# Kernel tuning notes

Measured on AMD Instinct MI355X. Metric: run time of the kernel, lower is better.

Reference implementation:

```python
import jax, jax.numpy as jnp
import numpy as np

EPS = 1e-12  # F.normalize default eps (norm clamped to at least eps)


def setup_inputs() -> dict:
    key = jax.random.key(0)
    k1, k2, k3, k4 = jax.random.split(key, 4)
    B, Cin, Cout, H, W = 8, 128, 32, 256, 256
    x = jax.random.normal(k1, (B, Cin, H, W), dtype=jnp.float32)
    qk = jax.random.normal(k2, (B, 2 * Cout, H, W), dtype=jnp.float32)
    # 1x1 conv params (PyTorch Conv2d default init scale ~ 1/sqrt(fan_in))
    w_v = jax.random.normal(k3, (Cout, Cin), dtype=jnp.float32) / np.sqrt(Cin)
    b_v = jax.random.normal(k4, (Cout,), dtype=jnp.float32) / np.sqrt(Cin)
    temperature = jnp.ones((1, 1, 1), dtype=jnp.float32)
    return {"x": x, "qk": qk, "w_v": w_v, "b_v": b_v, "temperature": temperature}


def reference(x, qk, w_v, b_v, temperature):
    B, Cin, H, W = x.shape
    Co = w_v.shape[0]
    N = H * W
    # 1x1 conv == channel GEMM
    v = jnp.einsum('bchw,oc->bohw', x, w_v) + b_v[None, :, None, None]
    # split qk: k = first Co channels, q = last Co channels; head=1
    q = qk[:, Co:].reshape(B, 1, Co, N)
    k = qk[:, :Co].reshape(B, 1, Co, N)
    v = v.reshape(B, 1, Co, N)
    # L2-normalize over spatial dim (F.normalize: divide by max(norm, eps))
    q = q / jnp.maximum(jnp.linalg.norm(q, axis=-1, keepdims=True), EPS)
    k = k / jnp.maximum(jnp.linalg.norm(k, axis=-1, keepdims=True), EPS)
    # channel-wise (transposed) attention: [B,1,Co,Co]
    attn = jnp.einsum('bhcn,bhdn->bhcd', q, k) * temperature
    attn = jax.nn.softmax(attn, axis=-1)
    out = jnp.einsum('bhcd,bhdn->bhcn', attn, v)  # [B,1,Co,N]
    return out
```

## Files before the change

### kernel.cpp

```cpp
#include <hip/hip_runtime.h>
#include <hip/hip_bf16.h>
#include <math.h>

#define NB    8
#define CIN   128
#define CO    32
#define CH    64
#define NN    65536
#define CPB   512
#define GBLK  (NN/CPB)
#define TCOLS 128
#define NTILES (CPB/TCOLS)

typedef __attribute__((ext_vector_type(8))) short bf16x8;
typedef __attribute__((ext_vector_type(16))) float f32x16;

__device__ __forceinline__ short f2bf(float f) {
    union { __hip_bfloat16 h; short s; } u;
    u.h = __float2bfloat16(f);
    return u.s;
}
__device__ __forceinline__ float bf2f(short s) {
    union { __hip_bfloat16 h; short s; } u;
    u.s = s;
    return __bfloat162float(u.h);
}

__global__ __launch_bounds__(256) void gram_kernel(const float* __restrict__ qk,
                                                   float* __restrict__ part,
                                                   float* __restrict__ partsq) {
    __shared__ float smem[CH * TCOLS];
    float4* tile4 = (float4*)smem;

    const int b = blockIdx.y;
    const int blk = blockIdx.x;
    const int t = threadIdx.x;
    const int w = t >> 6;
    const int l = t & 63;
    const int c = l & 31;
    const int half = l >> 5;

    const float* qkb = qk + (size_t)b * CH * NN;
    const size_t colbase0 = (size_t)blk * CPB;

    const int lrow[8] = {  (t) >> 5, (t + 256) >> 5, (t + 512) >> 5, (t + 768) >> 5,
                           (t + 1024) >> 5, (t + 1280) >> 5, (t + 1536) >> 5, (t + 1792) >> 5 };
    const int lcol4 = t & 31;

    f32x16 acc = {};
    float sq[8] = {0.f, 0.f, 0.f, 0.f, 0.f, 0.f, 0.f, 0.f};

    float4 st[8];
#pragma unroll
    for (int k = 0; k < 8; ++k)
        st[k] = *(const float4*)(qkb + (size_t)lrow[k] * NN + colbase0 + lcol4 * 4);

#pragma unroll
    for (int tau = 0; tau < NTILES; ++tau) {
#pragma unroll
        for (int k = 0; k < 8; ++k) {
            float4 v = st[k];
            sq[k] = fmaf(v.x, v.x, sq[k]);
            sq[k] = fmaf(v.y, v.y, sq[k]);
            sq[k] = fmaf(v.z, v.z, sq[k]);
            sq[k] = fmaf(v.w, v.w, sq[k]);
            tile4[lrow[k] * 32 + (lcol4 ^ (lrow[k] & 7))] = v;
        }
        __syncthreads();

        if (tau + 1 < NTILES) {
            const size_t colbase = colbase0 + (size_t)(tau + 1) * TCOLS;
#pragma unroll
            for (int k = 0; k < 8; ++k)
                st[k] = *(const float4*)(qkb + (size_t)lrow[k] * NN + colbase + lcol4 * 4);
        }

#pragma unroll
        for (int ss = 0; ss < 2; ++ss) {
            const int s = 2 * w + ss;
            const int f0 = s * 4 + half * 2;
            const int qrow = CO + c;
            const int krow = c;
            const int sw = c & 7;
            float4 q0 = tile4[qrow * 32 + (f0 ^ sw)];
            float4 q1 = tile4[qrow * 32 + ((f0 + 1) ^ sw)];
            float4 k0 = tile4[krow * 32 + (f0 ^ sw)];
            float4 k1 = tile4[krow * 32 + ((f0 + 1) ^ sw)];

            float qf[8] = {q0.x, q0.y, q0.z, q0.w, q1.x, q1.y, q1.z, q1.w};
            float kf[8] = {k0.x, k0.y, k0.z, k0.w, k1.x, k1.y, k1.z, k1.w};

            bf16x8 ah, al, bh, bl;
#pragma unroll
            for (int j = 0; j < 8; ++j) {
                short hq = f2bf(qf[j]);
                ah[j] = hq;
                al[j] = f2bf(qf[j] - bf2f(hq));
                short hk = f2bf(kf[j]);
                bh[j] = hk;
                bl[j] = f2bf(kf[j] - bf2f(hk));
            }
            acc = __builtin_amdgcn_mfma_f32_32x32x16_bf16(ah, bh, acc, 0, 0, 0);
            acc = __builtin_amdgcn_mfma_f32_32x32x16_bf16(ah, bl, acc, 0, 0, 0);
            acc = __builtin_amdgcn_mfma_f32_32x32x16_bf16(al, bh, acc, 0, 0, 0);
        }
        __syncthreads();
    }

#pragma unroll
    for (int r = 0; r < 16; ++r) {
        int row = (r & 3) + 8 * (r >> 2) + 4 * half;
        smem[w * 1024 + row * 32 + c] = acc[r];
    }
#pragma unroll
    for (int k = 0; k < 8; ++k)
        smem[4096 + ((t >> 5) + 8 * k) * 32 + (t & 31)] = sq[k];
    __syncthreads();

    float* pp = part + ((size_t)b * GBLK + blk) * 1024;
#pragma unroll
    for (int j = 0; j < 4; ++j) {
        int idx = t + j * 256;
        pp[idx] = smem[idx] + smem[1024 + idx] + smem[2048 + idx] + smem[3072 + idx];
    }
    if (t < 64) {
        float s = 0.f;
#pragma unroll
        for (int i = 0; i < 32; ++i) s += smem[4096 + t * 32 + i];
        partsq[((size_t)b * GBLK + blk) * 64 + t] = s;
    }
}

__global__ __launch_bounds__(128) void reduce_kernel(const float* __restrict__ part,
                                                     const float* __restrict__ partsq,
                                                     float* __restrict__ Sred) {
    const int b = blockIdx.y;
    const int v = blockIdx.x * 64 + (threadIdx.x >> 1);
    const int h = threadIdx.x & 1;
    float s = 0.f;
    if (v < 1024) {
        const float* p = part + (size_t)b * GBLK * 1024 + v;
        for (int ch = h * (GBLK / 2); ch < (h + 1) * (GBLK / 2); ++ch)
            s += p[(size_t)ch * 1024];
    } else {
        const float* p = partsq + (size_t)b * GBLK * 64 + (v - 1024);
        for (int ch = h * (GBLK / 2); ch < (h + 1) * (GBLK / 2); ++ch)
            s += p[(size_t)ch * 64];
    }
    s += __shfl_xor(s, 1);
    if (h == 0) Sred[b * 1088 + v] = s;
}

__global__ __launch_bounds__(256) void attn_kernel(const float* __restrict__ Sred,
                                                   const float* __restrict__ w_v,
                                                   const float* __restrict__ b_v,
                                                   const float* __restrict__ temp,
                                                   float* __restrict__ Weff,
                                                   float* __restrict__ beff) {
    __shared__ float sS[1024];
    __shared__ float snorm[64];
    __shared__ float sA[1024];
    const int t = threadIdx.x;
    const int b = blockIdx.x;

    for (int i = t; i < 1024; i += 256) sS[i] = Sred[b * 1088 + i];
    if (t < 64) snorm[t] = fmaxf(sqrtf(Sred[b * 1088 + 1024 + t]), 1e-12f);
    __syncthreads();

    if (t < 32) {
        const float T = temp[0];
        const float qn = snorm[32 + t];
        float m = -1e30f;
        for (int d = 0; d < 32; ++d)
            m = fmaxf(m, sS[t * 32 + d] / (qn * snorm[d]) * T);
        float sum = 0.f;
        for (int d = 0; d < 32; ++d)
            sum += expf(sS[t * 32 + d] / (qn * snorm[d]) * T - m);
        const float inv = 1.f / sum;
        for (int d = 0; d < 32; ++d)
            sA[t * 32 + d] = expf(sS[t * 32 + d] / (qn * snorm[d]) * T - m) * inv;
    }
    __syncthreads();

    for (int idx = t; idx < CO * CIN; idx += 256) {
        int cc = idx >> 7;
        int ci = idx & 127;
        float s = 0.f;
#pragma unroll
        for (int d = 0; d < 32; ++d) s += sA[cc * 32 + d] * w_v[d * CIN + ci];
        Weff[(size_t)b * CO * CIN + idx] = s;
    }
    if (t < 32) {
        float s = 0.f;
#pragma unroll
        for (int d = 0; d < 32; ++d) s += sA[t * 32 + d] * b_v[d];
        beff[b * CO + t] = s;
    }
}

__global__ __launch_bounds__(256) void out_kernel(const float* __restrict__ x,
                                                  const float* __restrict__ Weff,
                                                  const float* __restrict__ beff,
                                                  float* __restrict__ out) {
    const int b = blockIdx.y;
    const int n0 = blockIdx.x * 512 + threadIdx.x * 2;
    const float* xb = x + (size_t)b * CIN * NN + n0;
    const float* Wb = Weff + (size_t)b * CO * CIN;
    const float* bb = beff + b * CO;

    float a0[CO], a1[CO];
#pragma unroll
    for (int o = 0; o < CO; ++o) { a0[o] = bb[o]; a1[o] = bb[o]; }

#pragma unroll 4
    for (int ci = 0; ci < CIN; ++ci) {
        float2 xv = *(const float2*)(xb + (size_t)ci * NN);
#pragma unroll
        for (int o = 0; o < CO; ++o) {
            float wv = Wb[o * CIN + ci];
            a0[o] = fmaf(wv, xv.x, a0[o]);
            a1[o] = fmaf(wv, xv.y, a1[o]);
        }
    }

    float* ob = out + (size_t)b * CO * NN + n0;
#pragma unroll
    for (int o = 0; o < CO; ++o) {
        float2 r;
        r.x = a0[o];
        r.y = a1[o];
        *(float2*)(ob + (size_t)o * NN) = r;
    }
}

extern "C" void kernel_launch(void* const* d_in, const int* in_sizes, int n_in,
                              void* d_out, int out_size, void* d_ws, size_t ws_size,
                              hipStream_t stream) {
    const float* x    = (const float*)d_in[0];
    const float* qk   = (const float*)d_in[1];
    const float* w_v  = (const float*)d_in[2];
    const float* b_v  = (const float*)d_in[3];
    const float* temp = (const float*)d_in[4];
    float* out = (float*)d_out;

    float* part   = (float*)d_ws;
    float* partsq = part + (size_t)NB * GBLK * 1024;
    float* Sred   = partsq + (size_t)NB * GBLK * 64;
    float* Weff   = Sred + (size_t)NB * 1088;
    float* beff   = Weff + (size_t)NB * CO * CIN;

    gram_kernel<<<dim3(GBLK, NB), 256, 0, stream>>>(qk, part, partsq);
    reduce_kernel<<<dim3(17, NB), 128, 0, stream>>>(part, partsq, Sred);
    attn_kernel<<<dim3(NB), 256, 0, stream>>>(Sred, w_v, b_v, temp, Weff, beff);
    out_kernel<<<dim3(NN / 512, NB), 256, 0, stream>>>(x, Weff, beff, out);
}
```

Measured before the change: 116.5 us.

## Compute output GEMM with split-bf16 MFMA instead of scalar FP32 FMAs

The attention kernel now stores the effective weight matrix as hi/lo bf16 pairs. The output kernel computes the 32x128 by 128xN channel GEMM with 32x32x16 bf16 MFMA instructions, using three products (hi*hi, hi*lo, lo*hi) to approximate FP32 accuracy. The goal is to take the FMA work off the vector ALUs so the kernel is bound by memory bandwidth. In exchange it adds per-element bf16 splitting of x in registers and slightly lower precision than true FP32.

```diff
diff --git a/kernel.cpp b/kernel.cpp
--- a/kernel.cpp
+++ b/kernel.cpp
@@ -155,7 +155,8 @@
                                                    const float* __restrict__ w_v,
                                                    const float* __restrict__ b_v,
                                                    const float* __restrict__ temp,
-                                                   float* __restrict__ Weff,
+                                                   unsigned short* __restrict__ Whi,
+                                                   unsigned short* __restrict__ Wlo,
                                                    float* __restrict__ beff) {
     __shared__ float sS[1024];
     __shared__ float snorm[64];
@@ -188,7 +189,10 @@
         float s = 0.f;
 #pragma unroll
         for (int d = 0; d < 32; ++d) s += sA[cc * 32 + d] * w_v[d * CIN + ci];
-        Weff[(size_t)b * CO * CIN + idx] = s;
+        short hi = f2bf(s);
+        short lo = f2bf(s - bf2f(hi));
+        Whi[(size_t)b * CO * CIN + idx] = (unsigned short)hi;
+        Wlo[(size_t)b * CO * CIN + idx] = (unsigned short)lo;
     }
     if (t < 32) {
         float s = 0.f;
@@ -199,37 +203,64 @@
 }
 
 __global__ __launch_bounds__(256) void out_kernel(const float* __restrict__ x,
-                                                  const float* __restrict__ Weff,
+                                                  const unsigned short* __restrict__ Whi,
+                                                  const unsigned short* __restrict__ Wlo,
                                                   const float* __restrict__ beff,
                                                   float* __restrict__ out) {
     const int b = blockIdx.y;
-    const int n0 = blockIdx.x * 512 + threadIdx.x * 2;
-    const float* xb = x + (size_t)b * CIN * NN + n0;
-    const float* Wb = Weff + (size_t)b * CO * CIN;
-    const float* bb = beff + b * CO;
-
-    float a0[CO], a1[CO];
-#pragma unroll
-    for (int o = 0; o < CO; ++o) { a0[o] = bb[o]; a1[o] = bb[o]; }
-
-#pragma unroll 4
-    for (int ci = 0; ci < CIN; ++ci) {
-        float2 xv = *(const float2*)(xb + (size_t)ci * NN);
-#pragma unroll
-        for (int o = 0; o < CO; ++o) {
-            float wv = Wb[o * CIN + ci];
-            a0[o] = fmaf(wv, xv.x, a0[o]);
-            a1[o] = fmaf(wv, xv.y, a1[o]);
-        }
-    }
-
-    float* ob = out + (size_t)b * CO * NN + n0;
-#pragma unroll
-    for (int o = 0; o < CO; ++o) {
-        float2 r;
-        r.x = a0[o];
-        r.y = a1[o];
-        *(float2*)(ob + (size_t)o * NN) = r;
+    const int t = threadIdx.x;
+    const int w = t >> 6;
+    const int l = t & 63;
+    const int c = l & 31;
+    const int half = l >> 5;
+
+    const float* xb = x + (size_t)b * CIN * NN;
+
+    bf16x8 ah[8], al[8];
+    {
+        const unsigned short* Wh = Whi + (size_t)b * CO * CIN + c * CIN + half * 8;
+        const unsigned short* Wl = Wlo + (size_t)b * CO * CIN + c * CIN + half * 8;
+#pragma unroll
+        for (int s = 0; s < 8; ++s) {
+            ah[s] = *(const bf16x8*)(Wh + s * 16);
+            al[s] = *(const bf16x8*)(Wl + s * 16);
+        }
+    }
+    float bias[16];
+    {
+        const float* bb = beff + b * CO;
+#pragma unroll
+        for (int r = 0; r < 16; ++r)
+            bias[r] = bb[(r & 3) + 8 * (r >> 2) + 4 * half];
+    }
+
+#pragma unroll
+    for (int tile = 0; tile < 4; ++tile) {
+        const int col = blockIdx.x * 512 + w * 128 + tile * 32 + c;
+        f32x16 acc = {};
+#pragma unroll
+        for (int s = 0; s < 8; ++s) {
+            const float* xp = xb + (size_t)(s * 16 + half * 8) * NN + col;
+            float xv[8];
+#pragma unroll
+            for (int j = 0; j < 8; ++j) xv[j] = xp[(size_t)j * NN];
+            bf16x8 bh, bl;
+#pragma unroll
+            for (int j = 0; j < 8; ++j) {
+                short h = f2bf(xv[j]);
+                bh[j] = h;
+                bl[j] = f2bf(xv[j] - bf2f(h));
+            }
+            acc = __builtin_amdgcn_mfma_f32_32x32x16_bf16(ah[s], bh, acc, 0, 0, 0);
+            acc = __builtin_amdgcn_mfma_f32_32x32x16_bf16(ah[s], bl, acc, 0, 0, 0);
+            acc = __builtin_amdgcn_mfma_f32_32x32x16_bf16(al[s], bh, acc, 0, 0, 0);
+        }
+        float* ob = out + (size_t)b * CO * NN + col;
+#pragma unroll
+        for (int r = 0; r < 16; ++r) {
+            int o = (r & 3) + 8 * (r >> 2) + 4 * half;
+            ob[(size_t)o * NN] = acc[r] + bias[r];
+        }
     }
 }
 
@@ -246,11 +277,12 @@
     float* part   = (float*)d_ws;
     float* partsq = part + (size_t)NB * GBLK * 1024;
     float* Sred   = partsq + (size_t)NB * GBLK * 64;
-    float* Weff   = Sred + (size_t)NB * 1088;
-    float* beff   = Weff + (size_t)NB * CO * CIN;
+    unsigned short* Whi = (unsigned short*)(Sred + (size_t)NB * 1088);
+    unsigned short* Wlo = Whi + (size_t)NB * CO * CIN;
+    float* beff   = (float*)(Wlo + (size_t)NB * CO * CIN);
 
     gram_kernel<<<dim3(GBLK, NB), 256, 0, stream>>>(qk, part, partsq);
     reduce_kernel<<<dim3(17, NB), 128, 0, stream>>>(part, partsq, Sred);
-    attn_kernel<<<dim3(NB), 256, 0, stream>>>(Sred, w_v, b_v, temp, Weff, beff);
-    out_kernel<<<dim3(NN / 512, NB), 256, 0, stream>>>(x, Weff, beff, out);
-}
+    attn_kernel<<<dim3(NB), 256, 0, stream>>>(Sred, w_v, b_v, temp, Whi, Wlo, beff);
+    out_kernel<<<dim3(NN / 512, NB), 256, 0, stream>>>(x, Whi, Wlo, beff, out);
+}
```

After: 121.1 us. +4.0%, slower.
